# Optimization experiments

Measured on AMD Instinct MI355X. Metric: run time of the kernel, lower is better.

## Reference

```python
import jax, jax.numpy as jnp
import numpy as np

B = 16384
H_CH = 64   # num_eegch
P = 5       # patches
D = 64      # num_projected_features
NH = 4      # num_heads
DH = 16     # qkv_len
L = 6       # num_layers
SCALE = DH ** (-0.5)


def _ln(x, g, b, eps=1e-5):
    m = jnp.mean(x, axis=-1, keepdims=True)
    v = jnp.mean(jnp.square(x - m), axis=-1, keepdims=True)
    return (x - m) * jax.lax.rsqrt(v + eps) * g + b


def setup_inputs() -> dict:
    key = jax.random.key(0)
    ks = jax.random.split(key, 24)
    s = 0.02
    return {
        "x": jax.random.normal(ks[0], (B, 1, H_CH, P * 25), dtype=jnp.float32),
        "proj_w": jax.random.normal(ks[1], (H_CH * 25, D), dtype=jnp.float32) * s,
        "proj_b": jnp.zeros((D,), jnp.float32),
        "cls_token": jax.random.normal(ks[2], (1, 1, D), dtype=jnp.float32),
        "pe": jax.random.normal(ks[3], (1, P + 1, 1), dtype=jnp.float32),
        "qkv_w": jax.random.normal(ks[4], (L, D, 3 * NH * DH), dtype=jnp.float32) * s,
        "qkv_b": jnp.zeros((L, 3 * NH * DH), jnp.float32),
        "out_w": jax.random.normal(ks[5], (L, NH * DH, D), dtype=jnp.float32) * s,
        "out_b": jnp.zeros((L, D), jnp.float32),
        "ln1_g": jnp.ones((L, D), jnp.float32),
        "ln1_b": jnp.zeros((L, D), jnp.float32),
        "ln2_g": jnp.ones((L, D), jnp.float32),
        "ln2_b": jnp.zeros((L, D), jnp.float32),
        "mlp_w1": jax.random.normal(ks[6], (L, D, 2 * D), dtype=jnp.float32) * s,
        "mlp_b1": jnp.zeros((L, 2 * D), jnp.float32),
        "mlp_w2": jax.random.normal(ks[7], (L, 2 * D, D), dtype=jnp.float32) * s,
        "mlp_b2": jnp.zeros((L, D), jnp.float32),
        "head_g": jnp.ones((D,), jnp.float32),
        "head_b": jnp.zeros((D,), jnp.float32),
        "head_w": jax.random.normal(ks[8], (D, 2), dtype=jnp.float32) * s,
        "head_bias": jnp.zeros((2,), jnp.float32),
    }


def reference(x, proj_w, proj_b, cls_token, pe, qkv_w, qkv_b, out_w, out_b,
              ln1_g, ln1_b, ln2_g, ln2_b, mlp_w1, mlp_b1, mlp_w2, mlp_b2,
              head_g, head_b, head_w, head_bias):
    b = x.shape[0]
    # patchify exactly like the torch reshape/transpose chain
    x = x.reshape(b, 1, H_CH, P, 25)
    x = jnp.swapaxes(x, 3, 4)                    # (b,1,h,25,p)
    x = x.reshape(b, H_CH * 25, P)
    x = jnp.swapaxes(x, 1, 2)                    # (b,p,h*25)
    x = x @ proj_w + proj_b                      # (b,p,D)
    cls = jnp.broadcast_to(cls_token, (b, 1, D))
    x = jnp.concatenate([cls, x], axis=1)        # (b,p+1,D)
    x = x + pe                                   # pe broadcasts over feature dim (repeat of last dim 1)
    S = P + 1
    for i in range(L):
        h = _ln(x, ln1_g[i], ln1_b[i])
        qkv = h @ qkv_w[i] + qkv_b[i]            # (b,S,3*NH*DH)
        q, k, v = jnp.split(qkv, 3, axis=-1)
        q = q.reshape(b, S, NH, DH).transpose(0, 2, 1, 3)
        k = k.reshape(b, S, NH, DH).transpose(0, 2, 1, 3)
        v = v.reshape(b, S, NH, DH).transpose(0, 2, 1, 3)
        att = jax.nn.softmax(jnp.einsum('bhsd,bhtd->bhst', q, k) * SCALE, axis=-1)
        o = jnp.einsum('bhst,bhtd->bhsd', att, v)
        o = o.transpose(0, 2, 1, 3).reshape(b, S, NH * DH)
        x = o @ out_w[i] + out_b[i] + x
        h2 = _ln(x, ln2_g[i], ln2_b[i])
        m = jax.nn.gelu(h2 @ mlp_w1[i] + mlp_b1[i], approximate=False)  # torch GELU = exact erf; dropout off (eval)
        x = m @ mlp_w2[i] + mlp_b2[i] + x
    cls_out = _ln(x[:, 0, :], head_g, head_b)    # dropout off (eval)
    return jax.nn.softmax(cls_out @ head_w + head_bias, axis=-1)
```

## Files before the change

kernel.cpp:

```cpp
#include <hip/hip_runtime.h>
#include <hip/hip_bf16.h>
#include <math.h>


#define B_TOT   16384
#define SEQ     6
#define NLAYER  6

typedef float f4 __attribute__((ext_vector_type(4)));
typedef float v4f __attribute__((ext_vector_type(4)));
typedef __bf16 v8bf __attribute__((ext_vector_type(8)));
typedef unsigned short us16;

#define PROJ_BLOCKS 640
#define ROWS_BLK    128
#define XSTR        28

__global__ __launch_bounds__(256) void proj_kernel(
    const float* __restrict__ xin, const float* __restrict__ Wp,
    const float* __restrict__ pb, const float* __restrict__ cls,
    const float* __restrict__ pe, float* __restrict__ x0)
{
    const int tid  = threadIdx.x;
    const int blk  = blockIdx.x;

    if (blk >= PROJ_BLOCKS) {
        const float pe0 = pe[0];
        const f4* cls4 = (const f4*)cls;
        f4 cv[16];
#pragma unroll
        for (int j = 0; j < 16; ++j) cv[j] = cls4[j] + pe0;
        int r0 = (blk - PROJ_BLOCKS) * 1024 + tid * 4;
#pragma unroll
        for (int rr = 0; rr < 4; ++rr) {
            f4* dst = (f4*)(x0 + (size_t)(r0 + rr) * 384);
#pragma unroll
            for (int j = 0; j < 16; ++j) dst[j] = cv[j];
        }
        return;
    }

    __shared__ float xlds[2][ROWS_BLK * XSTR];
    __shared__ float wlds[2][25 * 64];

    const int lane = tid & 63;
    const int wv   = tid >> 6;
    const int rg   = lane >> 3;
    const int cg   = lane & 7;
    const int brow0 = blk * ROWS_BLK;

    unsigned goff[13];
    unsigned loff[13];
#pragma unroll
    for (int j = 0; j < 13; ++j) {
        int flat = tid + j * 256;
        if (j < 12 || tid < 128) {
            int row  = flat / 25;
            int t    = flat - row * 25;
            int grow = brow0 + row;
            int smp  = grow / 5;
            int p    = grow - smp * 5;
            goff[j] = (unsigned)smp * 8000u + (unsigned)p * 25u + (unsigned)t;
            loff[j] = (unsigned)(row * XSTR + t);
        } else { goff[j] = 0u; loff[j] = 0u; }
    }

    const f4* Wp4 = (const f4*)Wp;

    f4 acc[4][2];
#pragma unroll
    for (int j = 0; j < 4; ++j) { acc[j][0] = (f4)0.f; acc[j][1] = (f4)0.f; }

    float xg[13];
    f4    wg[2];

    {
#pragma unroll
        for (int j = 0; j < 12; ++j) xg[j] = xin[goff[j]];
        if (tid < 128) xg[12] = xin[goff[12]];
        wg[0] = Wp4[tid];
        if (tid < 144) wg[1] = Wp4[256 + tid];
#pragma unroll
        for (int j = 0; j < 12; ++j) xlds[0][loff[j]] = xg[j];
        if (tid < 128) xlds[0][loff[12]] = xg[12];
        ((f4*)wlds[0])[tid] = wg[0];
        if (tid < 144) ((f4*)wlds[0])[256 + tid] = wg[1];
    }
    __syncthreads();

    const int xbase = (wv * 32 + rg * 4) * XSTR;
    const int wcol  = cg * 8;

    for (int h = 0; h < 64; ++h) {
        const int bb = h & 1;
        if (h < 63) {
            const unsigned gadd = (unsigned)(h + 1) * 125u;
#pragma unroll
            for (int j = 0; j < 12; ++j) xg[j] = xin[goff[j] + gadd];
            if (tid < 128) xg[12] = xin[goff[12] + gadd];
            const f4* wsrc = Wp4 + (size_t)(h + 1) * 400;
            wg[0] = wsrc[tid];
            if (tid < 144) wg[1] = wsrc[256 + tid];
        }
        {
            const float* xw = &xlds[bb][xbase];
            const float* wb = &wlds[bb][wcol];
#pragma unroll
            for (int t4 = 0; t4 < 6; ++t4) {
                f4 xr[4];
#pragma unroll
                for (int j = 0; j < 4; ++j)
                    xr[j] = *(const f4*)&xw[j * XSTR + t4 * 4];
#pragma unroll
                for (int kk = 0; kk < 4; ++kk) {
                    const float* wrow = &wb[(t4 * 4 + kk) * 64];
                    f4 wa = *(const f4*)&wrow[0];
                    f4 wc = *(const f4*)&wrow[4];
#pragma unroll
                    for (int j = 0; j < 4; ++j) {
                        float xv = xr[j][kk];
                        acc[j][0] += xv * wa;
                        acc[j][1] += xv * wc;
                    }
                }
            }
            {
                const float* wrow = &wb[24 * 64];
                f4 wa = *(const f4*)&wrow[0];
                f4 wc = *(const f4*)&wrow[4];
#pragma unroll
                for (int j = 0; j < 4; ++j) {
                    float xv = xw[j * XSTR + 24];
                    acc[j][0] += xv * wa;
                    acc[j][1] += xv * wc;
                }
            }
        }
        if (h < 63) {
            const int nb = bb ^ 1;
#pragma unroll
            for (int j = 0; j < 12; ++j) xlds[nb][loff[j]] = xg[j];
            if (tid < 128) xlds[nb][loff[12]] = xg[12];
            ((f4*)wlds[nb])[tid] = wg[0];
            if (tid < 144) ((f4*)wlds[nb])[256 + tid] = wg[1];
        }
        __syncthreads();
    }

    const f4* pb4 = (const f4*)pb;
    const f4 pbv0 = pb4[cg * 2], pbv1 = pb4[cg * 2 + 1];
    const float peP[5] = {pe[1], pe[2], pe[3], pe[4], pe[5]};
#pragma unroll
    for (int j = 0; j < 4; ++j) {
        int grow = brow0 + wv * 32 + rg * 4 + j;
        int smp  = grow / 5;
        int p    = grow - smp * 5;
        float pev = peP[p];
        float* dst = x0 + ((size_t)smp * SEQ + (p + 1)) * 64 + cg * 8;
        *(f4*)dst       = acc[j][0] + pbv0 + pev;
        *(f4*)(dst + 4) = acc[j][1] + pbv1 + pev;
    }
}

#define PREP_TOT (6 * 98304)

__global__ __launch_bounds__(256) void prep_kernel(
    const float* __restrict__ qkv_w, const float* __restrict__ out_w,
    const float* __restrict__ mlp_w1, const float* __restrict__ mlp_w2,
    us16* __restrict__ Wext)
{
    int gid = blockIdx.x * 256 + threadIdx.x;
    if (gid >= PREP_TOT) return;
    int l = gid / 98304;
    int r = gid - l * 98304;
    int sec; float v;
    if (r < 36864) {
        int n = r / 192, k = r - n * 192; sec = k >> 6; int ks = k & 63;
        v = qkv_w[(size_t)(l * 64 + ks) * 192 + n];
    } else if (r < 49152) {
        int r2 = r - 36864; int n = r2 / 192, k = r2 - n * 192; sec = k >> 6; int ks = k & 63;
        v = out_w[(size_t)(l * 64 + ks) * 64 + n];
    } else if (r < 73728) {
        int r3 = r - 49152; int n = r3 / 192, k = r3 - n * 192; sec = k >> 6; int ks = k & 63;
        v = mlp_w1[(size_t)(l * 64 + ks) * 128 + n];
    } else {
        int r4 = r - 73728; int n = r4 / 384, k = r4 - n * 384; sec = k >> 7; int ks = k & 127;
        v = mlp_w2[(size_t)(l * 128 + ks) * 64 + n];
    }
    __bf16 hb = (__bf16)v;
    us16 u;
    if (sec < 2) u = __builtin_bit_cast(us16, hb);
    else {
        float rem = v - (float)hb;
        __bf16 lb = (__bf16)rem;
        u = __builtin_bit_cast(us16, lb);
    }
    Wext[gid] = u;
}

#define XS 68
#define HS 136
#define QS 196
#define MS 264

__device__ __forceinline__ float wred64(float v) {
#pragma unroll
    for (int o = 32; o > 0; o >>= 1) v += __shfl_xor(v, o, 64);
    return v;
}

__device__ __forceinline__ us16 bf_hi(float v) {
    __bf16 h = (__bf16)v; return __builtin_bit_cast(us16, h);
}
__device__ __forceinline__ us16 bf_lo(float v) {
    __bf16 h = (__bf16)v;
    float rem = v - (float)h;
    __bf16 l = (__bf16)rem;
    return __builtin_bit_cast(us16, l);
}

__device__ __forceinline__ void load_a_ke1(const us16* hp, int lane, v8bf a[3][6]) {
    const int g = lane >> 4;
#pragma unroll
    for (int mt = 0; mt < 3; ++mt) {
        int r  = mt * 16 + (lane & 15);
        int rx = r & 7;
        int rb = r * HS;
#pragma unroll
        for (int kt = 0; kt < 6; ++kt) {
            int sec = ((kt >> 1) == 1) ? 1 : 0;
            int c3  = ((kt & 1) << 2) + g;
            a[mt][kt] = *(const v8bf*)&hp[rb + sec * 64 + ((c3 ^ rx) << 3)];
        }
    }
}

__device__ __forceinline__ void ln_to_panel(const float* xp, us16* hp,
                                            const float* g_, const float* b_,
                                            int lane, int w) {
    f4 g4 = *(const f4*)&g_[(lane & 15) * 4];
    f4 b4 = *(const f4*)&b_[(lane & 15) * 4];
#pragma unroll
    for (int it = 0; it < 3; ++it) {
        int r = w * 12 + it * 4 + (lane >> 4);
        f4 xv = *(const f4*)&xp[r * XS + (lane & 15) * 4];
        float s = xv[0] + xv[1] + xv[2] + xv[3];
        s += __shfl_xor(s, 1, 64); s += __shfl_xor(s, 2, 64);
        s += __shfl_xor(s, 4, 64); s += __shfl_xor(s, 8, 64);
        float mean = s * (1.f / 64.f);
        f4 dv = xv - mean;
        float vs = dv[0]*dv[0] + dv[1]*dv[1] + dv[2]*dv[2] + dv[3]*dv[3];
        vs += __shfl_xor(vs, 1, 64); vs += __shfl_xor(vs, 2, 64);
        vs += __shfl_xor(vs, 4, 64); vs += __shfl_xor(vs, 8, 64);
        float rs = rsqrtf(vs * (1.f / 64.f) + 1e-5f);
        f4 h4 = dv * rs * g4 + b4;
        int C0 = (lane & 15) * 4;
        int chunk = C0 >> 3, e = C0 & 7;
        int ad = r * HS + ((chunk ^ (r & 7)) << 3) + e;
        ushort4 hi, lo;
        hi.x = bf_hi(h4[0]); hi.y = bf_hi(h4[1]); hi.z = bf_hi(h4[2]); hi.w = bf_hi(h4[3]);
        lo.x = bf_lo(h4[0]); lo.y = bf_lo(h4[1]); lo.z = bf_lo(h4[2]); lo.w = bf_lo(h4[3]);
        *(ushort4*)&hp[ad]      = hi;
        *(ushort4*)&hp[ad + 64] = lo;
    }
}

__global__ __launch_bounds__(256, 2) void tf2_kernel(
    const float* __restrict__ x0buf,
    const us16*  __restrict__ Wext,
    const float* __restrict__ qkv_b, const float* __restrict__ out_b,
    const float* __restrict__ ln1_g, const float* __restrict__ ln1_b,
    const float* __restrict__ ln2_g, const float* __restrict__ ln2_b,
    const float* __restrict__ mlp_b1, const float* __restrict__ mlp_b2,
    const float* __restrict__ head_g, const float* __restrict__ head_b,
    const float* __restrict__ head_w, const float* __restrict__ head_bias,
    float* __restrict__ out)
{
    __shared__ __align__(16) float x_lds[48 * XS];
    __shared__ __align__(16) us16  h_lds[48 * HS];
    __shared__ __align__(16) unsigned char u_buf[48 * MS * 2];
    __shared__ __align__(16) float att_lds[8 * 4 * 36];

    float* qkv_lds = (float*)u_buf;
    us16*  m_lds   = (us16*)u_buf;

    const int tid  = threadIdx.x;
    const int lane = tid & 63;
    const int w    = tid >> 6;
    const int bid  = blockIdx.x;

#pragma unroll
    for (int j = 0; j < 3; ++j) {
        int idx = tid + j * 256;
        int row = idx >> 4, c4 = idx & 15;
        *(f4*)&x_lds[row * XS + c4 * 4] =
            *(const f4*)&x0buf[((size_t)bid * 48 + row) * 64 + c4 * 4];
    }
    __syncthreads();

    for (int lay = 0; lay < NLAYER; ++lay) {
        const int lb = lay * 98304;

        ln_to_panel(x_lds, h_lds, ln1_g + lay * 64, ln1_b + lay * 64, lane, w);
        __syncthreads();

        {
            v8bf a[3][6];
            load_a_ke1(h_lds, lane, a);
            const us16* Bq = Wext + lb;
            const float* qb = qkv_b + lay * 192;
            const int g = lane >> 4;
#pragma unroll
            for (int ntl = 0; ntl < 3; ++ntl) {
                int nt = w * 3 + ntl;
                int C  = nt * 16 + (lane & 15);
                v4f acc0 = {0.f,0.f,0.f,0.f}, acc1 = acc0, acc2 = acc0;
#pragma unroll
                for (int kt = 0; kt < 6; ++kt) {
                    v8bf b = *(const v8bf*)&Bq[C * 192 + kt * 32 + g * 8];
                    acc0 = __builtin_amdgcn_mfma_f32_16x16x32_bf16(a[0][kt], b, acc0, 0, 0, 0);
                    acc1 = __builtin_amdgcn_mfma_f32_16x16x32_bf16(a[1][kt], b, acc1, 0, 0, 0);
                    acc2 = __builtin_amdgcn_mfma_f32_16x16x32_bf16(a[2][kt], b, acc2, 0, 0, 0);
                }
                float bias = qb[C];
#pragma unroll
                for (int reg = 0; reg < 4; ++reg) {
                    int rr = g * 4 + reg;
                    qkv_lds[(0 * 16 + rr) * QS + C]  = acc0[reg] + bias;
                    qkv_lds[(1 * 16 + rr) * QS + C]  = acc1[reg] + bias;
                    qkv_lds[(2 * 16 + rr) * QS + C]  = acc2[reg] + bias;
                }
            }
        }
        __syncthreads();

        if (tid < 192) {
            int a8 = tid / 24, rem = tid - a8 * 24;
            int hh = rem / 6, i = rem - hh * 6;
            int rb = a8 * 6;
            const float* qrow = &qkv_lds[(rb + i) * QS + hh * 16];
            f4 q0 = *(const f4*)&qrow[0],  q1 = *(const f4*)&qrow[4];
            f4 q2 = *(const f4*)&qrow[8],  q3 = *(const f4*)&qrow[12];
            float sc[6];
#pragma unroll
            for (int j = 0; j < 6; ++j) {
                const float* kr = &qkv_lds[(rb + j) * QS + 64 + hh * 16];
                f4 k0 = *(const f4*)&kr[0], k1 = *(const f4*)&kr[4];
                f4 k2 = *(const f4*)&kr[8], k3 = *(const f4*)&kr[12];
                f4 p = q0 * k0 + q1 * k1 + q2 * k2 + q3 * k3;
                sc[j] = (p[0] + p[1] + p[2] + p[3]) * 0.25f;
            }
            float mx = sc[0];
#pragma unroll
            for (int j = 1; j < 6; ++j) mx = fmaxf(mx, sc[j]);
            float e[6], sum = 0.f;
#pragma unroll
            for (int j = 0; j < 6; ++j) { e[j] = expf(sc[j] - mx); sum += e[j]; }
            float inv = 1.f / sum;
            float* ap = &att_lds[((a8 * 4 + hh) * 6 + i) * 6];
#pragma unroll
            for (int j = 0; j < 6; ++j) ap[j] = e[j] * inv;
        }
        __syncthreads();

        {
            int cg = tid & 15, rgrp = tid >> 4;
            int hh = cg >> 2;
#pragma unroll
            for (int k = 0; k < 3; ++k) {
                int r = rgrp + 16 * k;
                int a8 = r / 6, i = r - a8 * 6;
                int rb = a8 * 6;
                const float* ap = &att_lds[((a8 * 4 + hh) * 6 + i) * 6];
                f4 o = {0.f,0.f,0.f,0.f};
#pragma unroll
                for (int j = 0; j < 6; ++j)
                    o += ap[j] * *(const f4*)&qkv_lds[(rb + j) * QS + 128 + cg * 4];
                int C0 = cg * 4;
                int chunk = C0 >> 3, e = C0 & 7;
                int ad = r * HS + ((chunk ^ (r & 7)) << 3) + e;
                ushort4 hi, lo;
                hi.x = bf_hi(o[0]); hi.y = bf_hi(o[1]); hi.z = bf_hi(o[2]); hi.w = bf_hi(o[3]);
                lo.x = bf_lo(o[0]); lo.y = bf_lo(o[1]); lo.z = bf_lo(o[2]); lo.w = bf_lo(o[3]);
                *(ushort4*)&h_lds[ad]      = hi;
                *(ushort4*)&h_lds[ad + 64] = lo;
            }
        }
        __syncthreads();

        {
            v8bf a[3][6];
            load_a_ke1(h_lds, lane, a);
            const us16* Bo = Wext + lb + 36864;
            const int g = lane >> 4;
            int C = w * 16 + (lane & 15);
            v4f acc0 = {0.f,0.f,0.f,0.f}, acc1 = acc0, acc2 = acc0;
#pragma unroll
            for (int kt = 0; kt < 6; ++kt) {
                v8bf b = *(const v8bf*)&Bo[C * 192 + kt * 32 + g * 8];
                acc0 = __builtin_amdgcn_mfma_f32_16x16x32_bf16(a[0][kt], b, acc0, 0, 0, 0);
                acc1 = __builtin_amdgcn_mfma_f32_16x16x32_bf16(a[1][kt], b, acc1, 0, 0, 0);
                acc2 = __builtin_amdgcn_mfma_f32_16x16x32_bf16(a[2][kt], b, acc2, 0, 0, 0);
            }
            float bias = out_b[lay * 64 + C];
#pragma unroll
            for (int reg = 0; reg < 4; ++reg) {
                int rr = g * 4 + reg;
                x_lds[(0 * 16 + rr) * XS + C] += acc0[reg] + bias;
                x_lds[(1 * 16 + rr) * XS + C] += acc1[reg] + bias;
                x_lds[(2 * 16 + rr) * XS + C] += acc2[reg] + bias;
            }
        }
        __syncthreads();

        ln_to_panel(x_lds, h_lds, ln2_g + lay * 64, ln2_b + lay * 64, lane, w);
        __syncthreads();

        {
            v8bf a[3][6];
            load_a_ke1(h_lds, lane, a);
            const us16* B1 = Wext + lb + 49152;
            const float* b1 = mlp_b1 + lay * 128;
            const int g = lane >> 4;
#pragma unroll
            for (int q = 0; q < 2; ++q) {
                int nt = w * 2 + q;
                int C  = nt * 16 + (lane & 15);
                v4f acc0 = {0.f,0.f,0.f,0.f}, acc1 = acc0, acc2 = acc0;
#pragma unroll
                for (int kt = 0; kt < 6; ++kt) {
                    v8bf b = *(const v8bf*)&B1[C * 192 + kt * 32 + g * 8];
                    acc0 = __builtin_amdgcn_mfma_f32_16x16x32_bf16(a[0][kt], b, acc0, 0, 0, 0);
                    acc1 = __builtin_amdgcn_mfma_f32_16x16x32_bf16(a[1][kt], b, acc1, 0, 0, 0);
                    acc2 = __builtin_amdgcn_mfma_f32_16x16x32_bf16(a[2][kt], b, acc2, 0, 0, 0);
                }
                float bias = b1[C];
                int ch4 = C >> 3, e = C & 7;
#pragma unroll
                for (int mt = 0; mt < 3; ++mt) {
                    v4f acc = (mt == 0) ? acc0 : ((mt == 1) ? acc1 : acc2);
#pragma unroll
                    for (int reg = 0; reg < 4; ++reg) {
                        int row = mt * 16 + g * 4 + reg;
                        float u = acc[reg] + bias;
                        float gl = 0.5f * u * (1.f + erff(u * 0.70710678118654752f));
                        int ad = row * MS + ((ch4 ^ (row & 7)) << 3) + e;
                        m_lds[ad]       = bf_hi(gl);
                        m_lds[ad + 128] = bf_lo(gl);
                    }
                }
            }
        }
        __syncthreads();

        {
            v8bf a[3][12];
            const int g = lane >> 4;
#pragma unroll
            for (int mt = 0; mt < 3; ++mt) {
                int r  = mt * 16 + (lane & 15);
                int rx = r & 7;
                int rb = r * MS;
#pragma unroll
                for (int kt = 0; kt < 12; ++kt) {
                    int sec = (kt >> 2);
                    int off = (sec == 1) ? 128 : 0;
                    int c4  = ((kt & 3) << 2) + g;
                    a[mt][kt] = *(const v8bf*)&m_lds[rb + off + ((c4 ^ rx) << 3)];
                }
            }
            const us16* B2 = Wext + lb + 73728;
            int C = w * 16 + (lane & 15);
            v4f acc0 = {0.f,0.f,0.f,0.f}, acc1 = acc0, acc2 = acc0;
#pragma unroll
            for (int kt = 0; kt < 12; ++kt) {
                v8bf b = *(const v8bf*)&B2[C * 384 + kt * 32 + g * 8];
                acc0 = __builtin_amdgcn_mfma_f32_16x16x32_bf16(a[0][kt], b, acc0, 0, 0, 0);
                acc1 = __builtin_amdgcn_mfma_f32_16x16x32_bf16(a[1][kt], b, acc1, 0, 0, 0);
                acc2 = __builtin_amdgcn_mfma_f32_16x16x32_bf16(a[2][kt], b, acc2, 0, 0, 0);
            }
            float bias = mlp_b2[lay * 64 + C];
#pragma unroll
            for (int reg = 0; reg < 4; ++reg) {
                int rr = g * 4 + reg;
                x_lds[(0 * 16 + rr) * XS + C] += acc0[reg] + bias;
                x_lds[(1 * 16 + rr) * XS + C] += acc1[reg] + bias;
                x_lds[(2 * 16 + rr) * XS + C] += acc2[reg] + bias;
            }
        }
        __syncthreads();
    }

#pragma unroll
    for (int si = 0; si < 2; ++si) {
        int s = w * 2 + si;
        float val = x_lds[(s * 6) * XS + lane];
        float m  = wred64(val) * (1.f / 64.f);
        float dv = val - m;
        float var = wred64(dv * dv) * (1.f / 64.f);
        float hh  = dv * rsqrtf(var + 1e-5f) * head_g[lane] + head_b[lane];
        float l0  = wred64(hh * head_w[lane * 2 + 0]);
        float l1  = wred64(hh * head_w[lane * 2 + 1]);
        if (lane == 0) {
            l0 += head_bias[0];
            l1 += head_bias[1];
            float mx = fmaxf(l0, l1);
            float e0 = expf(l0 - mx), e1 = expf(l1 - mx);
            float inv = 1.f / (e0 + e1);
            out[(size_t)(bid * 8 + s) * 2 + 0] = e0 * inv;
            out[(size_t)(bid * 8 + s) * 2 + 1] = e1 * inv;
        }
    }
}

extern "C" void kernel_launch(void* const* d_in, const int* in_sizes, int n_in,
                              void* d_out, int out_size, void* d_ws, size_t ws_size,
                              hipStream_t stream) {
    const float* xin     = (const float*)d_in[0];
    const float* proj_w  = (const float*)d_in[1];
    const float* proj_b  = (const float*)d_in[2];
    const float* cls     = (const float*)d_in[3];
    const float* pe      = (const float*)d_in[4];
    const float* qkv_w   = (const float*)d_in[5];
    const float* qkv_b   = (const float*)d_in[6];
    const float* out_w   = (const float*)d_in[7];
    const float* out_b   = (const float*)d_in[8];
    const float* ln1_g   = (const float*)d_in[9];
    const float* ln1_b   = (const float*)d_in[10];
    const float* ln2_g   = (const float*)d_in[11];
    const float* ln2_b   = (const float*)d_in[12];
    const float* mlp_w1  = (const float*)d_in[13];
    const float* mlp_b1  = (const float*)d_in[14];
    const float* mlp_w2  = (const float*)d_in[15];
    const float* mlp_b2  = (const float*)d_in[16];
    const float* head_g  = (const float*)d_in[17];
    const float* head_b  = (const float*)d_in[18];
    const float* head_w  = (const float*)d_in[19];
    const float* head_bs = (const float*)d_in[20];
    float* outp = (float*)d_out;

    float* x0   = (float*)d_ws;
    us16*  Wext = (us16*)((char*)d_ws + 25165824);

    prep_kernel<<<(PREP_TOT + 255) / 256, 256, 0, stream>>>(
        qkv_w, out_w, mlp_w1, mlp_w2, Wext);

    proj_kernel<<<PROJ_BLOCKS + 16, 256, 0, stream>>>(
        xin, proj_w, proj_b, cls, pe, x0);

    tf2_kernel<<<B_TOT / 8, 256, 0, stream>>>(
        x0, Wext, qkv_b, out_b, ln1_g, ln1_b, ln2_g, ln2_b,
        mlp_b1, mlp_b2, head_g, head_b, head_w, head_bs, outp);
}
```

Measured before the change: 1.360 ms.

## Move patch projection onto bf16 MFMA with hi/lo split-precision operands

Replaces the FP32 FMA patch-projection GEMM with an MFMA-based kernel that splits inputs and weights into bf16 high and low parts. The products hi*hi, lo*hi and hi*lo approximate FP32 accuracy. The projection weights are pre-converted into a padded, MFMA-friendly layout inside the existing prep kernel. This targets the FP32 ALU cost of the 1600x64 projection over 81920 rows. It adds per-element bf16 conversion of activations, some padding waste (25 to 32 in K), and a small accuracy change.

```diff
diff --git a/kernel.cpp b/kernel.cpp
--- a/kernel.cpp
+++ b/kernel.cpp
@@ -11,203 +11,6 @@
 typedef float v4f __attribute__((ext_vector_type(4)));
 typedef __bf16 v8bf __attribute__((ext_vector_type(8)));
 typedef unsigned short us16;
-
-#define PROJ_BLOCKS 640
-#define ROWS_BLK    128
-#define XSTR        28
-
-__global__ __launch_bounds__(256) void proj_kernel(
-    const float* __restrict__ xin, const float* __restrict__ Wp,
-    const float* __restrict__ pb, const float* __restrict__ cls,
-    const float* __restrict__ pe, float* __restrict__ x0)
-{
-    const int tid  = threadIdx.x;
-    const int blk  = blockIdx.x;
-
-    if (blk >= PROJ_BLOCKS) {
-        const float pe0 = pe[0];
-        const f4* cls4 = (const f4*)cls;
-        f4 cv[16];
-#pragma unroll
-        for (int j = 0; j < 16; ++j) cv[j] = cls4[j] + pe0;
-        int r0 = (blk - PROJ_BLOCKS) * 1024 + tid * 4;
-#pragma unroll
-        for (int rr = 0; rr < 4; ++rr) {
-            f4* dst = (f4*)(x0 + (size_t)(r0 + rr) * 384);
-#pragma unroll
-            for (int j = 0; j < 16; ++j) dst[j] = cv[j];
-        }
-        return;
-    }
-
-    __shared__ float xlds[2][ROWS_BLK * XSTR];
-    __shared__ float wlds[2][25 * 64];
-
-    const int lane = tid & 63;
-    const int wv   = tid >> 6;
-    const int rg   = lane >> 3;
-    const int cg   = lane & 7;
-    const int brow0 = blk * ROWS_BLK;
-
-    unsigned goff[13];
-    unsigned loff[13];
-#pragma unroll
-    for (int j = 0; j < 13; ++j) {
-        int flat = tid + j * 256;
-        if (j < 12 || tid < 128) {
-            int row  = flat / 25;
-            int t    = flat - row * 25;
-            int grow = brow0 + row;
-            int smp  = grow / 5;
-            int p    = grow - smp * 5;
-            goff[j] = (unsigned)smp * 8000u + (unsigned)p * 25u + (unsigned)t;
-            loff[j] = (unsigned)(row * XSTR + t);
-        } else { goff[j] = 0u; loff[j] = 0u; }
-    }
-
-    const f4* Wp4 = (const f4*)Wp;
-
-    f4 acc[4][2];
-#pragma unroll
-    for (int j = 0; j < 4; ++j) { acc[j][0] = (f4)0.f; acc[j][1] = (f4)0.f; }
-
-    float xg[13];
-    f4    wg[2];
-
-    {
-#pragma unroll
-        for (int j = 0; j < 12; ++j) xg[j] = xin[goff[j]];
-        if (tid < 128) xg[12] = xin[goff[12]];
-        wg[0] = Wp4[tid];
-        if (tid < 144) wg[1] = Wp4[256 + tid];
-#pragma unroll
-        for (int j = 0; j < 12; ++j) xlds[0][loff[j]] = xg[j];
-        if (tid < 128) xlds[0][loff[12]] = xg[12];
-        ((f4*)wlds[0])[tid] = wg[0];
-        if (tid < 144) ((f4*)wlds[0])[256 + tid] = wg[1];
-    }
-    __syncthreads();
-
-    const int xbase = (wv * 32 + rg * 4) * XSTR;
-    const int wcol  = cg * 8;
-
-    for (int h = 0; h < 64; ++h) {
-        const int bb = h & 1;
-        if (h < 63) {
-            const unsigned gadd = (unsigned)(h + 1) * 125u;
-#pragma unroll
-            for (int j = 0; j < 12; ++j) xg[j] = xin[goff[j] + gadd];
-            if (tid < 128) xg[12] = xin[goff[12] + gadd];
-            const f4* wsrc = Wp4 + (size_t)(h + 1) * 400;
-            wg[0] = wsrc[tid];
-            if (tid < 144) wg[1] = wsrc[256 + tid];
-        }
-        {
-            const float* xw = &xlds[bb][xbase];
-            const float* wb = &wlds[bb][wcol];
-#pragma unroll
-            for (int t4 = 0; t4 < 6; ++t4) {
-                f4 xr[4];
-#pragma unroll
-                for (int j = 0; j < 4; ++j)
-                    xr[j] = *(const f4*)&xw[j * XSTR + t4 * 4];
-#pragma unroll
-                for (int kk = 0; kk < 4; ++kk) {
-                    const float* wrow = &wb[(t4 * 4 + kk) * 64];
-                    f4 wa = *(const f4*)&wrow[0];
-                    f4 wc = *(const f4*)&wrow[4];
-#pragma unroll
-                    for (int j = 0; j < 4; ++j) {
-                        float xv = xr[j][kk];
-                        acc[j][0] += xv * wa;
-                        acc[j][1] += xv * wc;
-                    }
-                }
-            }
-            {
-                const float* wrow = &wb[24 * 64];
-                f4 wa = *(const f4*)&wrow[0];
-                f4 wc = *(const f4*)&wrow[4];
-#pragma unroll
-                for (int j = 0; j < 4; ++j) {
-                    float xv = xw[j * XSTR + 24];
-                    acc[j][0] += xv * wa;
-                    acc[j][1] += xv * wc;
-                }
-            }
-        }
-        if (h < 63) {
-            const int nb = bb ^ 1;
-#pragma unroll
-            for (int j = 0; j < 12; ++j) xlds[nb][loff[j]] = xg[j];
-            if (tid < 128) xlds[nb][loff[12]] = xg[12];
-            ((f4*)wlds[nb])[tid] = wg[0];
-            if (tid < 144) ((f4*)wlds[nb])[256 + tid] = wg[1];
-        }
-        __syncthreads();
-    }
-
-    const f4* pb4 = (const f4*)pb;
-    const f4 pbv0 = pb4[cg * 2], pbv1 = pb4[cg * 2 + 1];
-    const float peP[5] = {pe[1], pe[2], pe[3], pe[4], pe[5]};
-#pragma unroll
-    for (int j = 0; j < 4; ++j) {
-        int grow = brow0 + wv * 32 + rg * 4 + j;
-        int smp  = grow / 5;
-        int p    = grow - smp * 5;
-        float pev = peP[p];
-        float* dst = x0 + ((size_t)smp * SEQ + (p + 1)) * 64 + cg * 8;
-        *(f4*)dst       = acc[j][0] + pbv0 + pev;
-        *(f4*)(dst + 4) = acc[j][1] + pbv1 + pev;
-    }
-}
-
-#define PREP_TOT (6 * 98304)
-
-__global__ __launch_bounds__(256) void prep_kernel(
-    const float* __restrict__ qkv_w, const float* __restrict__ out_w,
-    const float* __restrict__ mlp_w1, const float* __restrict__ mlp_w2,
-    us16* __restrict__ Wext)
-{
-    int gid = blockIdx.x * 256 + threadIdx.x;
-    if (gid >= PREP_TOT) return;
-    int l = gid / 98304;
-    int r = gid - l * 98304;
-    int sec; float v;
-    if (r < 36864) {
-        int n = r / 192, k = r - n * 192; sec = k >> 6; int ks = k & 63;
-        v = qkv_w[(size_t)(l * 64 + ks) * 192 + n];
-    } else if (r < 49152) {
-        int r2 = r - 36864; int n = r2 / 192, k = r2 - n * 192; sec = k >> 6; int ks = k & 63;
-        v = out_w[(size_t)(l * 64 + ks) * 64 + n];
-    } else if (r < 73728) {
-        int r3 = r - 49152; int n = r3 / 192, k = r3 - n * 192; sec = k >> 6; int ks = k & 63;
-        v = mlp_w1[(size_t)(l * 64 + ks) * 128 + n];
-    } else {
-        int r4 = r - 73728; int n = r4 / 384, k = r4 - n * 384; sec = k >> 7; int ks = k & 127;
-        v = mlp_w2[(size_t)(l * 128 + ks) * 64 + n];
-    }
-    __bf16 hb = (__bf16)v;
-    us16 u;
-    if (sec < 2) u = __builtin_bit_cast(us16, hb);
-    else {
-        float rem = v - (float)hb;
-        __bf16 lb = (__bf16)rem;
-        u = __builtin_bit_cast(us16, lb);
-    }
-    Wext[gid] = u;
-}
-
-#define XS 68
-#define HS 136
-#define QS 196
-#define MS 264
-
-__device__ __forceinline__ float wred64(float v) {
-#pragma unroll
-    for (int o = 32; o > 0; o >>= 1) v += __shfl_xor(v, o, 64);
-    return v;
-}
 
 __device__ __forceinline__ us16 bf_hi(float v) {
     __bf16 h = (__bf16)v; return __builtin_bit_cast(us16, h);
@@ -217,6 +20,200 @@
     float rem = v - (float)h;
     __bf16 l = (__bf16)rem;
     return __builtin_bit_cast(us16, l);
+}
+
+#define PB2 1280
+
+__global__ __launch_bounds__(256) void proj2_kernel(
+    const float* __restrict__ xin,
+    const us16*  __restrict__ Wpx,
+    const float* __restrict__ pb,
+    const float* __restrict__ cls,
+    const float* __restrict__ pe,
+    float* __restrict__ x0)
+{
+    const int tid = threadIdx.x;
+    const int blk = blockIdx.x;
+
+    if (blk >= PB2) {
+        const float pe0 = pe[0];
+        const f4* cls4 = (const f4*)cls;
+        f4 cv[16];
+#pragma unroll
+        for (int j = 0; j < 16; ++j) cv[j] = cls4[j] + pe0;
+        int r0 = (blk - PB2) * 1024 + tid * 4;
+#pragma unroll
+        for (int rr = 0; rr < 4; ++rr) {
+            f4* dst = (f4*)(x0 + (size_t)(r0 + rr) * 384);
+#pragma unroll
+            for (int j = 0; j < 16; ++j) dst[j] = cv[j];
+        }
+        return;
+    }
+
+    __shared__ __align__(16) us16 xpan[2][64 * 64];
+
+    const int lane = tid & 63;
+    const int w    = tid >> 6;
+    const int c    = lane & 15;
+    const int g    = lane >> 4;
+    const int brow0 = blk * 64;
+
+    unsigned gb[2];
+    int      q_[2];
+    unsigned ahi[2], alo[2];
+#pragma unroll
+    for (int j = 0; j < 2; ++j) {
+        int idx = tid + j * 256;
+        int row = idx >> 3, q = idx & 7;
+        int grow = brow0 + row;
+        int smp = grow / 5;
+        int p   = grow - smp * 5;
+        gb[j] = (unsigned)smp * 8000u + (unsigned)p * 25u + (unsigned)(q * 4);
+        q_[j] = q;
+        int ch_hi = q >> 1;
+        int ch_lo = (q >> 1) + 4;
+        ahi[j] = (unsigned)(row * 64 + (((ch_hi ^ (row & 7))) << 3) + (q & 1) * 4);
+        alo[j] = (unsigned)(row * 64 + (((ch_lo ^ (row & 7))) << 3) + (q & 1) * 4);
+    }
+
+    v4f acc[4];
+#pragma unroll
+    for (int mt = 0; mt < 4; ++mt) acc[mt] = (v4f){0.f, 0.f, 0.f, 0.f};
+
+    {
+#pragma unroll
+        for (int j = 0; j < 2; ++j) {
+            float v[4];
+#pragma unroll
+            for (int e = 0; e < 4; ++e) {
+                int t = q_[j] * 4 + e;
+                v[e] = (t < 25) ? xin[gb[j] + e] : 0.f;
+            }
+            ushort4 hv, lv;
+            hv.x = bf_hi(v[0]); hv.y = bf_hi(v[1]); hv.z = bf_hi(v[2]); hv.w = bf_hi(v[3]);
+            lv.x = bf_lo(v[0]); lv.y = bf_lo(v[1]); lv.z = bf_lo(v[2]); lv.w = bf_lo(v[3]);
+            *(ushort4*)&xpan[0][ahi[j]] = hv;
+            *(ushort4*)&xpan[0][alo[j]] = lv;
+        }
+    }
+    __syncthreads();
+
+    const us16* Bn = Wpx + (size_t)(w * 16 + c) * 6144;
+    const int achunk[3] = { g, 4 + g, g };
+
+    for (int h = 0; h < 64; ++h) {
+        const int bb = h & 1;
+        float vn[2][4];
+        if (h < 63) {
+            const unsigned gadd = (unsigned)(h + 1) * 125u;
+#pragma unroll
+            for (int j = 0; j < 2; ++j) {
+#pragma unroll
+                for (int e = 0; e < 4; ++e) {
+                    int t = q_[j] * 4 + e;
+                    vn[j][e] = (t < 25) ? xin[gb[j] + gadd + e] : 0.f;
+                }
+            }
+        }
+
+        v8bf bfr[3];
+#pragma unroll
+        for (int s = 0; s < 3; ++s)
+            bfr[s] = *(const v8bf*)&Bn[h * 96 + s * 32 + g * 8];
+
+        const us16* xp = xpan[bb];
+#pragma unroll
+        for (int mt = 0; mt < 4; ++mt) {
+            int r  = mt * 16 + c;
+            int rb = r * 64;
+            int rx = r & 7;
+#pragma unroll
+            for (int s = 0; s < 3; ++s) {
+                v8bf a = *(const v8bf*)&xp[rb + ((achunk[s] ^ rx) << 3)];
+                acc[mt] = __builtin_amdgcn_mfma_f32_16x16x32_bf16(a, bfr[s], acc[mt], 0, 0, 0);
+            }
+        }
+
+        if (h < 63) {
+            const int nb = bb ^ 1;
+#pragma unroll
+            for (int j = 0; j < 2; ++j) {
+                ushort4 hv, lv;
+                hv.x = bf_hi(vn[j][0]); hv.y = bf_hi(vn[j][1]); hv.z = bf_hi(vn[j][2]); hv.w = bf_hi(vn[j][3]);
+                lv.x = bf_lo(vn[j][0]); lv.y = bf_lo(vn[j][1]); lv.z = bf_lo(vn[j][2]); lv.w = bf_lo(vn[j][3]);
+                *(ushort4*)&xpan[nb][ahi[j]] = hv;
+                *(ushort4*)&xpan[nb][alo[j]] = lv;
+            }
+        }
+        __syncthreads();
+    }
+
+    const int col = w * 16 + c;
+    const float pbv = pb[col];
+    const float peP[5] = {pe[1], pe[2], pe[3], pe[4], pe[5]};
+#pragma unroll
+    for (int mt = 0; mt < 4; ++mt) {
+#pragma unroll
+        for (int reg = 0; reg < 4; ++reg) {
+            int grow = brow0 + mt * 16 + g * 4 + reg;
+            int smp  = grow / 5;
+            int p    = grow - smp * 5;
+            x0[((size_t)smp * SEQ + (p + 1)) * 64 + col] = acc[mt][reg] + pbv + peP[p];
+        }
+    }
+}
+
+#define PREP_TF   (6 * 98304)
+#define PREP_TOT  (PREP_TF + 393216)
+
+__global__ __launch_bounds__(256) void prep_kernel(
+    const float* __restrict__ qkv_w, const float* __restrict__ out_w,
+    const float* __restrict__ mlp_w1, const float* __restrict__ mlp_w2,
+    const float* __restrict__ proj_w,
+    us16* __restrict__ Wext, us16* __restrict__ Wpx)
+{
+    int gid = blockIdx.x * 256 + threadIdx.x;
+    if (gid < PREP_TF) {
+        int l = gid / 98304;
+        int r = gid - l * 98304;
+        int sec; float v;
+        if (r < 36864) {
+            int n = r / 192, k = r - n * 192; sec = k >> 6; int ks = k & 63;
+            v = qkv_w[(size_t)(l * 64 + ks) * 192 + n];
+        } else if (r < 49152) {
+            int r2 = r - 36864; int n = r2 / 192, k = r2 - n * 192; sec = k >> 6; int ks = k & 63;
+            v = out_w[(size_t)(l * 64 + ks) * 64 + n];
+        } else if (r < 73728) {
+            int r3 = r - 49152; int n = r3 / 192, k = r3 - n * 192; sec = k >> 6; int ks = k & 63;
+            v = mlp_w1[(size_t)(l * 64 + ks) * 128 + n];
+        } else {
+            int r4 = r - 73728; int n = r4 / 384, k = r4 - n * 384; sec = k >> 7; int ks = k & 127;
+            v = mlp_w2[(size_t)(l * 128 + ks) * 64 + n];
+        }
+        Wext[gid] = (sec < 2) ? bf_hi(v) : bf_lo(v);
+    } else {
+        int r = gid - PREP_TF;
+        int n   = r / 6144;
+        int rem = r - n * 6144;
+        int h   = rem / 96;
+        int kk  = rem - h * 96;
+        int sec = kk >> 5;
+        int k   = kk & 31;
+        float v = (k < 25) ? proj_w[(size_t)(h * 25 + k) * 64 + n] : 0.f;
+        Wpx[r] = (sec < 2) ? bf_hi(v) : bf_lo(v);
+    }
+}
+
+#define XS 68
+#define HS 136
+#define QS 196
+#define MS 264
+
+__device__ __forceinline__ float wred64(float v) {
+#pragma unroll
+    for (int o = 32; o > 0; o >>= 1) v += __shfl_xor(v, o, 64);
+    return v;
 }
 
 __device__ __forceinline__ void load_a_ke1(const us16* hp, int lane, v8bf a[3][6]) {
@@ -541,12 +538,13 @@
 
     float* x0   = (float*)d_ws;
     us16*  Wext = (us16*)((char*)d_ws + 25165824);
-
-    prep_kernel<<<(PREP_TOT + 255) / 256, 256, 0, stream>>>(
-        qkv_w, out_w, mlp_w1, mlp_w2, Wext);
-
-    proj_kernel<<<PROJ_BLOCKS + 16, 256, 0, stream>>>(
-        xin, proj_w, proj_b, cls, pe, x0);
+    us16*  Wpx  = (us16*)((char*)d_ws + 25165824 + 2359296);
+
+    prep_kernel<<<PREP_TOT / 256, 256, 0, stream>>>(
+        qkv_w, out_w, mlp_w1, mlp_w2, proj_w, Wext, Wpx);
+
+    proj2_kernel<<<PB2 + 16, 256, 0, stream>>>(
+        xin, Wpx, proj_b, cls, pe, x0);
 
     tf2_kernel<<<B_TOT / 8, 256, 0, stream>>>(
         x0, Wext, qkv_b, out_b, ln1_g, ln1_b, ln2_g, ln2_b,
```

New measurement: 1.222 ms. -10.2%, faster.
